# Optimization experiments

Measured on AMD Instinct MI355X. Metric: run time of the kernel, lower is better.

Reference implementation:

```python
import jax, jax.numpy as jnp
import numpy as np

B, N, F = 8, 1024, 256
OUT, REL = 256, 16
NADJ = 7  # ((2 relations + consecutive) * 2 for backward) + self link


def setup_inputs() -> dict:
    key = jax.random.key(0)
    k0, k1, k2, k3, k4 = jax.random.split(key, 5)
    features = jax.random.normal(k0, (B, N, F), dtype=jnp.float32)
    A1 = jax.random.uniform(k1, (B, N, N), dtype=jnp.float32)
    A2 = jax.random.uniform(k2, (B, N, N), dtype=jnp.float32)
    # learned params: one (F+REL, OUT) weight per adjacency matrix, edge embeddings init 'ones', bias (N, OUT)
    W = jax.random.normal(k3, (NADJ, F + REL, OUT), dtype=jnp.float32) * 0.05
    W_edges = jnp.ones((NADJ, REL), dtype=jnp.float32)
    b = jax.random.uniform(k4, (N, OUT), dtype=jnp.float32, minval=-0.05, maxval=0.05)
    return {"features": features, "A1": A1, "A2": A2, "W": W, "W_edges": W_edges, "b": b}


def reference(features, A1, A2, W, W_edges, b):
    # eye = A[0] * zeros(N) + eye(N)  -> batch-broadcast identity [B,N,N]
    eye = jnp.zeros_like(A1) + jnp.eye(N, dtype=A1.dtype)
    # original rolls along axis 0 (batch) of the broadcast identity (faithful replication)
    shifted = jnp.roll(eye, 1, axis=0)
    A_fwd = [A1, A2, shifted]                      # relations + consecutive link
    A_list = A_fwd + [jnp.swapaxes(a, 1, 2) for a in A_fwd]  # backward links
    A_list.append(eye)                             # self links
    A = jnp.stack(A_list, axis=0)                  # [R,B,N,N]

    # concat(features, tile(W_edges[r])) @ W[r] == features @ W[r][:F] + W_edges[r] @ W[r][F:]
    HW = jnp.einsum('bnf,rfo->rbno', features, W[:, :F]) \
         + jnp.einsum('rd,rdo->ro', W_edges, W[:, F:])[:, None, None, :]  # [R,B,N,OUT]
    AHW = jnp.einsum('rbnm,rbmo->rbno', A, HW)     # batched adjacency matmul
    out = jnp.max(AHW, axis=0) + b                 # max-aggregate over relations, add bias
    return out                                     # activation = linear
```

## Files before the change

kernel.cpp:

```cpp
#include <hip/hip_runtime.h>
#include <hip/hip_bf16.h>

#define B_ 8
#define N_ 1024
#define F_ 256
#define OUT_ 256
#define REL_ 16
#define NADJ_ 7

typedef __attribute__((ext_vector_type(8))) _Float16 f16x8;
typedef __attribute__((ext_vector_type(2))) _Float16 f16x2;
typedef __attribute__((ext_vector_type(4))) float f32x4;

__device__ __forceinline__ void gll16(const _Float16* g, _Float16* l) {
    __builtin_amdgcn_global_load_lds(
        (const __attribute__((address_space(1))) void*)g,
        (__attribute__((address_space(3))) void*)l, 16, 0, 0);
}

__constant__ const int c_perm[7] = {0, 1, 3, 4, 2, 5, 6};

__global__ __launch_bounds__(256) void prep_kernel(const float* __restrict__ W,
                                                   const float* __restrict__ We,
                                                   const float* __restrict__ feat,
                                                   float* __restrict__ cb,
                                                   _Float16* __restrict__ WTp,
                                                   _Float16* __restrict__ Fe) {
    int bid = blockIdx.x, tid = threadIdx.x;
    if (bid < 7) {
        int idx = bid * 256 + tid;
        int j = idx / OUT_, o = idx % OUT_;
        int r = c_perm[j];
        const float* Wr = W + (size_t)r * (F_ + REL_) * OUT_;
        float s = 0.f;
#pragma unroll
        for (int d = 0; d < REL_; ++d) s += We[r * REL_ + d] * Wr[(F_ + d) * OUT_ + o];
        cb[idx] = s;
    } else if (bid < 1799) {
        int idx = (bid - 7) * 256 + tid;
        int j = idx >> 16, rem = idx & 65535, o = rem >> 8, f = rem & 255;
        int r = c_perm[j];
        WTp[idx] = (_Float16)W[((size_t)r * (F_ + REL_) + f) * OUT_ + o];
    } else {
        int i = (bid - 1799) * 256 + tid;
        size_t base = (size_t)i * 8;
        float4 a = *(const float4*)(feat + base);
        float4 b = *(const float4*)(feat + base + 4);
        f16x8 v = {(_Float16)a.x, (_Float16)a.y, (_Float16)a.z, (_Float16)a.w,
                   (_Float16)b.x, (_Float16)b.y, (_Float16)b.z, (_Float16)b.w};
        *(f16x8*)(Fe + base) = v;
    }
}

__global__ __launch_bounds__(256) void hw7_kernel(const _Float16* __restrict__ Fe,
                                                  const _Float16* __restrict__ WTp,
                                                  const float* __restrict__ cb,
                                                  _Float16* __restrict__ HWT,
                                                  _Float16* __restrict__ HWN) {
    __shared__ _Float16 S[8192];
    const int bid = blockIdx.x, tid = threadIdx.x;
    const int z = bid / 128, rem = bid % 128, bx = rem & 63, by = rem >> 6;
    const bool tr = (z < 4);
    const _Float16* A  = tr ? (WTp + (size_t)z * 65536) : Fe;
    const _Float16* Bt = tr ? Fe : (WTp + (size_t)z * 65536);
    const int m0 = (tr ? by : bx) * 128;
    const int n0 = (tr ? bx : by) * 128;
    _Float16* As = S;
    _Float16* Bs = S + 4096;
    const int wave = tid >> 6, lane = tid & 63, lm = lane & 15, q = lane >> 4;
    const int wr = (wave >> 1) * 64, wc = (wave & 1) * 64;
    const int srow = tid >> 2, sk = (tid & 3) * 8;
    const _Float16* ga0 = A + (size_t)(m0 + srow) * F_ + sk;
    const _Float16* ga1 = ga0 + (size_t)64 * F_;
    const _Float16* gb0 = Bt + (size_t)(n0 + srow) * F_ + sk;
    const _Float16* gb1 = gb0 + (size_t)64 * F_;
    _Float16* la0 = As + tid * 8;
    _Float16* la1 = As + 2048 + tid * 8;
    _Float16* lb0 = Bs + tid * 8;
    _Float16* lb1 = Bs + 2048 + tid * 8;

    f32x4 acc[4][4] = {};
    for (int k0 = 0; k0 < F_; k0 += 32) {
        gll16(ga0 + k0, la0);
        gll16(ga1 + k0, la1);
        gll16(gb0 + k0, lb0);
        gll16(gb1 + k0, lb1);
        __syncthreads();
        f16x8 af[4], bf[4];
#pragma unroll
        for (int i = 0; i < 4; ++i) af[i] = *(const f16x8*)(As + (wr + i * 16 + lm) * 32 + q * 8);
#pragma unroll
        for (int j = 0; j < 4; ++j) bf[j] = *(const f16x8*)(Bs + (wc + j * 16 + lm) * 32 + q * 8);
#pragma unroll
        for (int i = 0; i < 4; ++i)
#pragma unroll
            for (int j = 0; j < 4; ++j)
                acc[i][j] = __builtin_amdgcn_mfma_f32_16x16x32_f16(af[i], bf[j], acc[i][j], 0, 0, 0);
        __syncthreads();
    }
    const float* cbz = cb + (size_t)z * 256;
    if (tr) {
        _Float16* C = HWT + (size_t)z * ((size_t)256 * 8192);
#pragma unroll
        for (int i = 0; i < 4; ++i)
#pragma unroll
            for (int j = 0; j < 4; ++j)
#pragma unroll
                for (int g = 0; g < 4; ++g) {
                    int row = wr + i * 16 + q * 4 + g;
                    int col = wc + j * 16 + lm;
                    float v = acc[i][j][g] + cbz[m0 + row];
                    C[(size_t)(m0 + row) * 8192 + (n0 + col)] = (_Float16)v;
                }
    } else {
        _Float16* C = HWN + (size_t)(z - 4) * ((size_t)8192 * 256);
#pragma unroll
        for (int i = 0; i < 4; ++i)
#pragma unroll
            for (int j = 0; j < 4; ++j)
#pragma unroll
                for (int g = 0; g < 4; ++g) {
                    int row = wr + i * 16 + q * 4 + g;
                    int col = wc + j * 16 + lm;
                    float v = acc[i][j][g] + cbz[n0 + col];
                    C[(size_t)(m0 + row) * 256 + (n0 + col)] = (_Float16)v;
                }
    }
}

__global__ __launch_bounds__(256) void p2_kernel(const float* __restrict__ A1,
                                                 const float* __restrict__ A2,
                                                 const _Float16* __restrict__ HWT,
                                                 _Float16* __restrict__ AHW) {
    __shared__ _Float16 As[128 * 32];
    __shared__ _Float16 Bs[128 * 32];
    const int d = blockIdx.x;
    const int member = (d >> 3) & 1;
    const int p = (d & 7) | ((d >> 4) << 3);
    const int mt = p & 7, zz = p >> 3;
    const int rr = zz >> 3, b = zz & 7;
    const _Float16* Bt = HWT + (size_t)rr * (256 * 8192) + (size_t)b * 1024;
    _Float16* C = AHW + (size_t)rr * (8 * 262144) + (size_t)b * 262144;
    const int m0 = mt * 128, n0 = member * 128;
    const int tid = threadIdx.x;
    const int wave = tid >> 6, lane = tid & 63, lm = lane & 15, q = lane >> 4;
    const int wr = (wave >> 1) * 64, wc = (wave & 1) * 64;
    const int srow = tid >> 2, sk = (tid & 3) * 8;
    const _Float16* gb0 = Bt + (size_t)(n0 + srow) * 8192 + sk;
    const _Float16* gb1 = gb0 + (size_t)64 * 8192;
    _Float16* lb0 = Bs + tid * 8;
    _Float16* lb1 = Bs + 2048 + tid * 8;
    const int swv = (tid >> 6) & 3;
    _Float16* la0 = As + (tid >> 2) * 32 + (((tid & 3) ^ swv) * 8);
    _Float16* la1 = la0 + 2048;

    const float* Ag = ((rr & 1) ? A2 : A1) + (size_t)b * N_ * N_;
    f32x4 acc[4][4] = {};
    if (rr < 2) {
        const float* Ag0 = Ag + (size_t)(m0 + srow) * N_ + sk;
        const float* Ag1 = Ag0 + (size_t)64 * N_;
        float4 pa0 = *(const float4*)(Ag0);
        float4 pa1 = *(const float4*)(Ag0 + 4);
        float4 pb0 = *(const float4*)(Ag1);
        float4 pb1 = *(const float4*)(Ag1 + 4);
        for (int k0 = 0; k0 < N_; k0 += 32) {
            f16x8 v0 = {(_Float16)pa0.x, (_Float16)pa0.y, (_Float16)pa0.z, (_Float16)pa0.w,
                        (_Float16)pa1.x, (_Float16)pa1.y, (_Float16)pa1.z, (_Float16)pa1.w};
            f16x8 v1 = {(_Float16)pb0.x, (_Float16)pb0.y, (_Float16)pb0.z, (_Float16)pb0.w,
                        (_Float16)pb1.x, (_Float16)pb1.y, (_Float16)pb1.z, (_Float16)pb1.w};
            *(f16x8*)la0 = v0;
            *(f16x8*)la1 = v1;
            gll16(gb0 + k0, lb0);
            gll16(gb1 + k0, lb1);
            if (k0 + 32 < N_) {
                pa0 = *(const float4*)(Ag0 + k0 + 32);
                pa1 = *(const float4*)(Ag0 + k0 + 36);
                pb0 = *(const float4*)(Ag1 + k0 + 32);
                pb1 = *(const float4*)(Ag1 + k0 + 36);
            }
            __syncthreads();
            f16x8 af[4], bf[4];
#pragma unroll
            for (int i = 0; i < 4; ++i)
                af[i] = *(const f16x8*)(As + (wr + i * 16 + lm) * 32 + ((q ^ i) * 8));
#pragma unroll
            for (int j = 0; j < 4; ++j)
                bf[j] = *(const f16x8*)(Bs + (wc + j * 16 + lm) * 32 + q * 8);
#pragma unroll
            for (int i = 0; i < 4; ++i)
#pragma unroll
                for (int j = 0; j < 4; ++j)
                    acc[i][j] = __builtin_amdgcn_mfma_f32_16x16x32_f16(af[i], bf[j], acc[i][j], 0, 0, 0);
            __syncthreads();
        }
    } else {
        const int kk = (tid >> 4) * 2, ms = (tid & 15) * 8;
        const int sw = (ms >> 4) & 3;
        _Float16* wp = As + ms * 32 + (kk ^ (sw << 3));
        const float* ga = Ag + (size_t)kk * N_ + m0 + ms;
        float4 pa0 = *(const float4*)(ga);
        float4 pa1 = *(const float4*)(ga + 4);
        float4 pb0 = *(const float4*)(ga + N_);
        float4 pb1 = *(const float4*)(ga + N_ + 4);
        for (int k0 = 0; k0 < N_; k0 += 32) {
            f16x2 w;
            w = f16x2{(_Float16)pa0.x, (_Float16)pb0.x}; *(f16x2*)(wp + 0 * 32) = w;
            w = f16x2{(_Float16)pa0.y, (_Float16)pb0.y}; *(f16x2*)(wp + 1 * 32) = w;
            w = f16x2{(_Float16)pa0.z, (_Float16)pb0.z}; *(f16x2*)(wp + 2 * 32) = w;
            w = f16x2{(_Float16)pa0.w, (_Float16)pb0.w}; *(f16x2*)(wp + 3 * 32) = w;
            w = f16x2{(_Float16)pa1.x, (_Float16)pb1.x}; *(f16x2*)(wp + 4 * 32) = w;
            w = f16x2{(_Float16)pa1.y, (_Float16)pb1.y}; *(f16x2*)(wp + 5 * 32) = w;
            w = f16x2{(_Float16)pa1.z, (_Float16)pb1.z}; *(f16x2*)(wp + 6 * 32) = w;
            w = f16x2{(_Float16)pa1.w, (_Float16)pb1.w}; *(f16x2*)(wp + 7 * 32) = w;
            gll16(gb0 + k0, lb0);
            gll16(gb1 + k0, lb1);
            if (k0 + 32 < N_) {
                ga += (size_t)32 * N_;
                pa0 = *(const float4*)(ga);
                pa1 = *(const float4*)(ga + 4);
                pb0 = *(const float4*)(ga + N_);
                pb1 = *(const float4*)(ga + N_ + 4);
            }
            __syncthreads();
            f16x8 af[4], bf[4];
#pragma unroll
            for (int i = 0; i < 4; ++i)
                af[i] = *(const f16x8*)(As + (wr + i * 16 + lm) * 32 + ((q ^ i) * 8));
#pragma unroll
            for (int j = 0; j < 4; ++j)
                bf[j] = *(const f16x8*)(Bs + (wc + j * 16 + lm) * 32 + q * 8);
#pragma unroll
            for (int i = 0; i < 4; ++i)
#pragma unroll
                for (int j = 0; j < 4; ++j)
                    acc[i][j] = __builtin_amdgcn_mfma_f32_16x16x32_f16(af[i], bf[j], acc[i][j], 0, 0, 0);
            __syncthreads();
        }
    }
#pragma unroll
    for (int i = 0; i < 4; ++i)
#pragma unroll
        for (int j = 0; j < 4; ++j)
#pragma unroll
            for (int g = 0; g < 4; ++g) {
                int row = wr + i * 16 + q * 4 + g;
                int col = wc + j * 16 + lm;
                C[(size_t)(m0 + row) * 256 + (n0 + col)] = (_Float16)acc[i][j][g];
            }
}

__global__ __launch_bounds__(256) void max_kernel(const _Float16* __restrict__ AHW,
                                                  const _Float16* __restrict__ HWN,
                                                  const float* __restrict__ bias,
                                                  float* __restrict__ out) {
    size_t i = ((size_t)blockIdx.x * 256 + threadIdx.x) * 8;
    const size_t slab = (size_t)B_ * N_ * OUT_;
    float m[8];
    f16x8 v = *(const f16x8*)(AHW + i);
#pragma unroll
    for (int e = 0; e < 8; ++e) m[e] = (float)v[e];
#pragma unroll
    for (int rr = 1; rr < 4; ++rr) {
        f16x8 w = *(const f16x8*)(AHW + rr * slab + i);
#pragma unroll
        for (int e = 0; e < 8; ++e) m[e] = fmaxf(m[e], (float)w[e]);
    }
#pragma unroll
    for (int j = 0; j < 3; ++j) {
        f16x8 w = *(const f16x8*)(HWN + j * slab + i);
#pragma unroll
        for (int e = 0; e < 8; ++e) m[e] = fmaxf(m[e], (float)w[e]);
    }
    size_t bidx = i & ((size_t)N_ * OUT_ - 1);
    float4 b0 = *(const float4*)(bias + bidx);
    float4 b1 = *(const float4*)(bias + bidx + 4);
    float4 o0 = {m[0] + b0.x, m[1] + b0.y, m[2] + b0.z, m[3] + b0.w};
    float4 o1 = {m[4] + b1.x, m[5] + b1.y, m[6] + b1.z, m[7] + b1.w};
    *(float4*)(out + i) = o0;
    *(float4*)(out + i + 4) = o1;
}

__global__ void cbias_kernel(const float* __restrict__ W, const float* __restrict__ We,
                             float* __restrict__ c) {
    int idx = blockIdx.x * 256 + threadIdx.x;
    if (idx >= NADJ_ * OUT_) return;
    int r = idx / OUT_, o = idx % OUT_;
    const float* Wr = W + (size_t)r * (F_ + REL_) * OUT_;
    float s = 0.f;
#pragma unroll
    for (int d = 0; d < REL_; ++d) s += We[r * REL_ + d] * Wr[(F_ + d) * OUT_ + o];
    c[idx] = s;
}

__global__ __launch_bounds__(256) void hw_kernel(const float* __restrict__ feat,
                                                 const float* __restrict__ W,
                                                 const float* __restrict__ cb,
                                                 _Float16* __restrict__ HWb) {
    __shared__ _Float16 As[64][32];
    __shared__ _Float16 Bs[64][32];
    const int mt = blockIdx.x, ct = blockIdx.y;
    const int tid = threadIdx.x, wave = tid >> 6, lane = tid & 63;
    const int r = (ct * 64) / OUT_;
    const int o0 = (ct * 64) % OUT_;
    const float* Bg = W + (size_t)r * (F_ + REL_) * OUT_ + o0;
    const int m0 = mt * 64;
    const int lm = lane & 15, q = lane >> 4;
    f32x4 acc[4] = {};
    for (int k0 = 0; k0 < F_; k0 += 32) {
        {
            int seg = (tid & 3) * 8, m = tid >> 2;
            const float* src = feat + (size_t)(m0 + m) * F_ + k0 + seg;
#pragma unroll
            for (int j = 0; j < 8; ++j) As[m][seg + j] = (_Float16)src[j];
        }
        {
            int kk = tid >> 3, ns = (tid & 7) * 8;
            const float* src = Bg + (size_t)(k0 + kk) * OUT_ + ns;
#pragma unroll
            for (int j = 0; j < 8; ++j) Bs[ns + j][kk] = (_Float16)src[j];
        }
        __syncthreads();
        f16x8 a = *(const f16x8*)&As[wave * 16 + lm][q * 8];
#pragma unroll
        for (int c4 = 0; c4 < 4; ++c4) {
            f16x8 b = *(const f16x8*)&Bs[c4 * 16 + lm][q * 8];
            acc[c4] = __builtin_amdgcn_mfma_f32_16x16x32_f16(a, b, acc[c4], 0, 0, 0);
        }
        __syncthreads();
    }
#pragma unroll
    for (int c4 = 0; c4 < 4; ++c4)
#pragma unroll
        for (int g = 0; g < 4; ++g) {
            int row = wave * 16 + (lane >> 4) * 4 + g;
            int col = c4 * 16 + lm;
            float v = acc[c4][g] + cb[r * OUT_ + o0 + col];
            HWb[((size_t)r * B_ * N_ + m0 + row) * OUT_ + o0 + col] = (_Float16)v;
        }
}

__global__ __launch_bounds__(256) void agg_kernel(const float* __restrict__ A1,
                                                  const float* __restrict__ A2,
                                                  const _Float16* __restrict__ HWb,
                                                  const float* __restrict__ bias,
                                                  float* __restrict__ out) {
    __shared__ _Float16 As[64][32];
    __shared__ _Float16 Bs[64][32];
    const int b = blockIdx.z, nt = blockIdx.y, ot = blockIdx.x;
    const int tid = threadIdx.x, wave = tid >> 6, lane = tid & 63;
    const int n0 = nt * 64, o0 = ot * 64;
    const int lm = lane & 15, q = lane >> 4;
    const size_t rstride = (size_t)B_ * N_ * OUT_;
    f32x4 mx[4];
#pragma unroll
    for (int i = 0; i < 4; ++i) mx[i] = f32x4{-1e30f, -1e30f, -1e30f, -1e30f};
#pragma unroll 1
    for (int rr = 0; rr < 4; ++rr) {
        const float* Ag = ((rr & 1) ? A2 : A1) + (size_t)b * N_ * N_;
        const bool tr = (rr >= 2);
        const int r = (rr < 2) ? rr : rr + 1;
        const _Float16* Bg = HWb + (size_t)r * rstride + (size_t)b * N_ * OUT_ + o0;
        f32x4 acc[4] = {};
        for (int k0 = 0; k0 < N_; k0 += 32) {
            if (!tr) {
                int seg = (tid & 3) * 8, m = tid >> 2;
                const float* src = Ag + (size_t)(n0 + m) * N_ + k0 + seg;
#pragma unroll
                for (int j = 0; j < 8; ++j) As[m][seg + j] = (_Float16)src[j];
            } else {
                int kk = tid >> 3, ms = (tid & 7) * 8;
                const float* src = Ag + (size_t)(k0 + kk) * N_ + n0 + ms;
#pragma unroll
                for (int j = 0; j < 8; ++j) As[ms + j][kk] = (_Float16)src[j];
            }
            {
                int kk = tid >> 3, ns = (tid & 7) * 8;
                const _Float16* src = Bg + (size_t)(k0 + kk) * OUT_ + ns;
#pragma unroll
                for (int j = 0; j < 8; ++j) Bs[ns + j][kk] = src[j];
            }
            __syncthreads();
            f16x8 a = *(const f16x8*)&As[wave * 16 + lm][q * 8];
#pragma unroll
            for (int c4 = 0; c4 < 4; ++c4) {
                f16x8 bb = *(const f16x8*)&Bs[c4 * 16 + lm][q * 8];
                acc[c4] = __builtin_amdgcn_mfma_f32_16x16x32_f16(a, bb, acc[c4], 0, 0, 0);
            }
            __syncthreads();
        }
#pragma unroll
        for (int c4 = 0; c4 < 4; ++c4)
#pragma unroll
            for (int g = 0; g < 4; ++g) mx[c4][g] = fmaxf(mx[c4][g], acc[c4][g]);
    }
#pragma unroll
    for (int c4 = 0; c4 < 4; ++c4)
#pragma unroll
        for (int g = 0; g < 4; ++g) {
            int row = wave * 16 + (lane >> 4) * 4 + g;
            int col = c4 * 16 + lm;
            size_t pos = ((size_t)b * N_ + n0 + row) * OUT_ + o0 + col;
            float v = mx[c4][g];
            v = fmaxf(v, (float)HWb[2 * rstride + pos]);
            v = fmaxf(v, (float)HWb[5 * rstride + pos]);
            v = fmaxf(v, (float)HWb[6 * rstride + pos]);
            out[pos] = v + bias[((size_t)(n0 + row)) * OUT_ + o0 + col];
        }
}

extern "C" void kernel_launch(void* const* d_in, const int* in_sizes, int n_in,
                              void* d_out, int out_size, void* d_ws, size_t ws_size,
                              hipStream_t stream) {
    const float* feat = (const float*)d_in[0];
    const float* A1   = (const float*)d_in[1];
    const float* A2   = (const float*)d_in[2];
    const float* W    = (const float*)d_in[3];
    const float* We   = (const float*)d_in[4];
    const float* bias = (const float*)d_in[5];
    float* out = (float*)d_out;

    const size_t OFF_CB   = 0;
    const size_t OFF_WT   = 8192;
    const size_t OFF_FE   = 1048576;
    const size_t OFF_HWT  = 5242880;
    const size_t OFF_HWN  = 22020096;
    const size_t OFF_AHW  = 34603008;
    const size_t WS_NEEDED = 51380224;

    if (ws_size >= WS_NEEDED) {
        float*    cbp = (float*)((char*)d_ws + OFF_CB);
        _Float16* WTp = (_Float16*)((char*)d_ws + OFF_WT);
        _Float16* Fe  = (_Float16*)((char*)d_ws + OFF_FE);
        _Float16* HWT = (_Float16*)((char*)d_ws + OFF_HWT);
        _Float16* HWN = (_Float16*)((char*)d_ws + OFF_HWN);
        _Float16* AHW = (_Float16*)((char*)d_ws + OFF_AHW);

        prep_kernel<<<2823, 256, 0, stream>>>(W, We, feat, cbp, WTp, Fe);
        hw7_kernel<<<896, 256, 0, stream>>>(Fe, WTp, cbp, HWT, HWN);
        p2_kernel<<<512, 256, 0, stream>>>(A1, A2, HWT, AHW);
        max_kernel<<<1024, 256, 0, stream>>>(AHW, HWN, bias, out);
    } else {
        float* cb = (float*)d_ws;
        _Float16* HWb = (_Float16*)((char*)d_ws + 8192);
        cbias_kernel<<<7, 256, 0, stream>>>(W, We, cb);
        hw_kernel<<<dim3(128, 28), 256, 0, stream>>>(feat, W, cb, HWb);
        agg_kernel<<<dim3(4, 16, 8), 256, 0, stream>>>(A1, A2, HWb, bias, out);
    }
}
```

Baseline: 188.7 us.

## Split-K the adjacency matmul into two halves and sum partials in max kernel

The p2 aggregation GEMM is split along K into two 512-wide halves, doubling the grid from 512 to 1024 blocks so the GPU's compute units are better filled. Each iteration now stages 64 K-columns in two LDS sub-buffers, halving the number of barriers per unit of work. Partial results go to a second AHW slab, and the max kernel adds the two partials before taking the max, which costs extra fp16 workspace traffic and rounds each partial to fp16 separately. The workspace requirement grows, so the fast path falls back to the slow path if the workspace is too small.

```diff
diff --git a/kernel.cpp b/kernel.cpp
--- a/kernel.cpp
+++ b/kernel.cpp
@@ -9,6 +9,7 @@
 #define NADJ_ 7
 
 typedef __attribute__((ext_vector_type(8))) _Float16 f16x8;
+typedef __attribute__((ext_vector_type(4))) _Float16 f16x4;
 typedef __attribute__((ext_vector_type(2))) _Float16 f16x2;
 typedef __attribute__((ext_vector_type(4))) float f32x4;
 
@@ -16,6 +17,11 @@
     __builtin_amdgcn_global_load_lds(
         (const __attribute__((address_space(1))) void*)g,
         (__attribute__((address_space(3))) void*)l, 16, 0, 0);
+}
+
+__device__ __forceinline__ f16x8 cvt8(float4 a, float4 b) {
+    return f16x8{(_Float16)a.x, (_Float16)a.y, (_Float16)a.z, (_Float16)a.w,
+                 (_Float16)b.x, (_Float16)b.y, (_Float16)b.z, (_Float16)b.w};
 }
 
 __constant__ const int c_perm[7] = {0, 1, 3, 4, 2, 5, 6};
@@ -46,9 +52,7 @@
         size_t base = (size_t)i * 8;
         float4 a = *(const float4*)(feat + base);
         float4 b = *(const float4*)(feat + base + 4);
-        f16x8 v = {(_Float16)a.x, (_Float16)a.y, (_Float16)a.z, (_Float16)a.w,
-                   (_Float16)b.x, (_Float16)b.y, (_Float16)b.z, (_Float16)b.w};
-        *(f16x8*)(Fe + base) = v;
+        *(f16x8*)(Fe + base) = cvt8(a, b);
     }
 }
 
@@ -132,108 +136,123 @@
                                                  const float* __restrict__ A2,
                                                  const _Float16* __restrict__ HWT,
                                                  _Float16* __restrict__ AHW) {
-    __shared__ _Float16 As[128 * 32];
-    __shared__ _Float16 Bs[128 * 32];
+    __shared__ _Float16 As[2 * 4096];
+    __shared__ _Float16 Bs[2 * 4096];
     const int d = blockIdx.x;
-    const int member = (d >> 3) & 1;
-    const int p = (d & 7) | ((d >> 4) << 3);
-    const int mt = p & 7, zz = p >> 3;
+    const int xcd = d & 7, slot = d >> 3;
+    const int Ghi = xcd + 8 * (slot >> 4);
+    const int member = (slot >> 3) & 1;
+    const int mt = slot & 7;
+    const int kh = Ghi & 1;
+    const int zz = Ghi >> 1;
     const int rr = zz >> 3, b = zz & 7;
+
+    const size_t slab = (size_t)B_ * N_ * OUT_;
     const _Float16* Bt = HWT + (size_t)rr * (256 * 8192) + (size_t)b * 1024;
-    _Float16* C = AHW + (size_t)rr * (8 * 262144) + (size_t)b * 262144;
-    const int m0 = mt * 128, n0 = member * 128;
+    _Float16* C = AHW + (size_t)kh * (4 * slab) + (size_t)rr * slab + (size_t)b * (N_ * OUT_);
+    const int m0 = mt * 128, n0 = member * 128, kbase = kh * 512;
     const int tid = threadIdx.x;
     const int wave = tid >> 6, lane = tid & 63, lm = lane & 15, q = lane >> 4;
     const int wr = (wave >> 1) * 64, wc = (wave & 1) * 64;
     const int srow = tid >> 2, sk = (tid & 3) * 8;
-    const _Float16* gb0 = Bt + (size_t)(n0 + srow) * 8192 + sk;
+    const _Float16* gb0 = Bt + (size_t)(n0 + srow) * 8192 + kbase + sk;
     const _Float16* gb1 = gb0 + (size_t)64 * 8192;
     _Float16* lb0 = Bs + tid * 8;
     _Float16* lb1 = Bs + 2048 + tid * 8;
-    const int swv = (tid >> 6) & 3;
-    _Float16* la0 = As + (tid >> 2) * 32 + (((tid & 3) ^ swv) * 8);
-    _Float16* la1 = la0 + 2048;
+    _Float16* la0 = As + srow * 32 + (((tid & 3) ^ ((tid >> 6) & 3)) * 8);
 
     const float* Ag = ((rr & 1) ? A2 : A1) + (size_t)b * N_ * N_;
     f32x4 acc[4][4] = {};
-    if (rr < 2) {
-        const float* Ag0 = Ag + (size_t)(m0 + srow) * N_ + sk;
-        const float* Ag1 = Ag0 + (size_t)64 * N_;
-        float4 pa0 = *(const float4*)(Ag0);
-        float4 pa1 = *(const float4*)(Ag0 + 4);
-        float4 pb0 = *(const float4*)(Ag1);
-        float4 pb1 = *(const float4*)(Ag1 + 4);
-        for (int k0 = 0; k0 < N_; k0 += 32) {
-            f16x8 v0 = {(_Float16)pa0.x, (_Float16)pa0.y, (_Float16)pa0.z, (_Float16)pa0.w,
-                        (_Float16)pa1.x, (_Float16)pa1.y, (_Float16)pa1.z, (_Float16)pa1.w};
-            f16x8 v1 = {(_Float16)pb0.x, (_Float16)pb0.y, (_Float16)pb0.z, (_Float16)pb0.w,
-                        (_Float16)pb1.x, (_Float16)pb1.y, (_Float16)pb1.z, (_Float16)pb1.w};
-            *(f16x8*)la0 = v0;
-            *(f16x8*)la1 = v1;
-            gll16(gb0 + k0, lb0);
-            gll16(gb1 + k0, lb1);
-            if (k0 + 32 < N_) {
-                pa0 = *(const float4*)(Ag0 + k0 + 32);
-                pa1 = *(const float4*)(Ag0 + k0 + 36);
-                pb0 = *(const float4*)(Ag1 + k0 + 32);
-                pb1 = *(const float4*)(Ag1 + k0 + 36);
-            }
-            __syncthreads();
+
+    auto domfma = [&]() {
+#pragma unroll
+        for (int u2 = 0; u2 < 2; ++u2) {
+            const _Float16* Au = As + u2 * 4096;
+            const _Float16* Bu = Bs + u2 * 4096;
             f16x8 af[4], bf[4];
 #pragma unroll
             for (int i = 0; i < 4; ++i)
-                af[i] = *(const f16x8*)(As + (wr + i * 16 + lm) * 32 + ((q ^ i) * 8));
+                af[i] = *(const f16x8*)(Au + (wr + i * 16 + lm) * 32 + ((q ^ i) * 8));
 #pragma unroll
             for (int j = 0; j < 4; ++j)
-                bf[j] = *(const f16x8*)(Bs + (wc + j * 16 + lm) * 32 + q * 8);
+                bf[j] = *(const f16x8*)(Bu + (wc + j * 16 + lm) * 32 + q * 8);
 #pragma unroll
             for (int i = 0; i < 4; ++i)
 #pragma unroll
                 for (int j = 0; j < 4; ++j)
                     acc[i][j] = __builtin_amdgcn_mfma_f32_16x16x32_f16(af[i], bf[j], acc[i][j], 0, 0, 0);
+        }
+    };
+
+    if (rr < 2) {
+        const float* Ag0 = Ag + (size_t)(m0 + srow) * N_ + kbase + sk;
+        const float* Ag1 = Ag0 + (size_t)64 * N_;
+        float4 r0a = *(const float4*)(Ag0);
+        float4 r0b = *(const float4*)(Ag0 + 4);
+        float4 r1a = *(const float4*)(Ag0 + 32);
+        float4 r1b = *(const float4*)(Ag0 + 36);
+        float4 r2a = *(const float4*)(Ag1);
+        float4 r2b = *(const float4*)(Ag1 + 4);
+        float4 r3a = *(const float4*)(Ag1 + 32);
+        float4 r3b = *(const float4*)(Ag1 + 36);
+        for (int t = 0; t < 8; ++t) {
+            gll16(gb0 + t * 64, lb0);
+            gll16(gb0 + t * 64 + 32, lb0 + 4096);
+            gll16(gb1 + t * 64, lb1);
+            gll16(gb1 + t * 64 + 32, lb1 + 4096);
+            *(f16x8*)(la0)        = cvt8(r0a, r0b);
+            *(f16x8*)(la0 + 4096) = cvt8(r1a, r1b);
+            *(f16x8*)(la0 + 2048) = cvt8(r2a, r2b);
+            *(f16x8*)(la0 + 6144) = cvt8(r3a, r3b);
+            if (t < 7) {
+                const float* p0 = Ag0 + (t + 1) * 64;
+                const float* p1 = Ag1 + (t + 1) * 64;
+                r0a = *(const float4*)(p0);      r0b = *(const float4*)(p0 + 4);
+                r1a = *(const float4*)(p0 + 32); r1b = *(const float4*)(p0 + 36);
+                r2a = *(const float4*)(p1);      r2b = *(const float4*)(p1 + 4);
+                r3a = *(const float4*)(p1 + 32); r3b = *(const float4*)(p1 + 36);
+            }
+            __syncthreads();
+            domfma();
             __syncthreads();
         }
     } else {
-        const int kk = (tid >> 4) * 2, ms = (tid & 15) * 8;
-        const int sw = (ms >> 4) & 3;
-        _Float16* wp = As + ms * 32 + (kk ^ (sw << 3));
-        const float* ga = Ag + (size_t)kk * N_ + m0 + ms;
-        float4 pa0 = *(const float4*)(ga);
-        float4 pa1 = *(const float4*)(ga + 4);
-        float4 pb0 = *(const float4*)(ga + N_);
-        float4 pb1 = *(const float4*)(ga + N_ + 4);
-        for (int k0 = 0; k0 < N_; k0 += 32) {
-            f16x2 w;
-            w = f16x2{(_Float16)pa0.x, (_Float16)pb0.x}; *(f16x2*)(wp + 0 * 32) = w;
-            w = f16x2{(_Float16)pa0.y, (_Float16)pb0.y}; *(f16x2*)(wp + 1 * 32) = w;
-            w = f16x2{(_Float16)pa0.z, (_Float16)pb0.z}; *(f16x2*)(wp + 2 * 32) = w;
-            w = f16x2{(_Float16)pa0.w, (_Float16)pb0.w}; *(f16x2*)(wp + 3 * 32) = w;
-            w = f16x2{(_Float16)pa1.x, (_Float16)pb1.x}; *(f16x2*)(wp + 4 * 32) = w;
-            w = f16x2{(_Float16)pa1.y, (_Float16)pb1.y}; *(f16x2*)(wp + 5 * 32) = w;
-            w = f16x2{(_Float16)pa1.z, (_Float16)pb1.z}; *(f16x2*)(wp + 6 * 32) = w;
-            w = f16x2{(_Float16)pa1.w, (_Float16)pb1.w}; *(f16x2*)(wp + 7 * 32) = w;
-            gll16(gb0 + k0, lb0);
-            gll16(gb1 + k0, lb1);
-            if (k0 + 32 < N_) {
-                ga += (size_t)32 * N_;
-                pa0 = *(const float4*)(ga);
-                pa1 = *(const float4*)(ga + 4);
-                pb0 = *(const float4*)(ga + N_);
-                pb1 = *(const float4*)(ga + N_ + 4);
-            }
-            __syncthreads();
-            f16x8 af[4], bf[4];
-#pragma unroll
-            for (int i = 0; i < 4; ++i)
-                af[i] = *(const f16x8*)(As + (wr + i * 16 + lm) * 32 + ((q ^ i) * 8));
-#pragma unroll
-            for (int j = 0; j < 4; ++j)
-                bf[j] = *(const f16x8*)(Bs + (wc + j * 16 + lm) * 32 + q * 8);
-#pragma unroll
-            for (int i = 0; i < 4; ++i)
-#pragma unroll
-                for (int j = 0; j < 4; ++j)
-                    acc[i][j] = __builtin_amdgcn_mfma_f32_16x16x32_f16(af[i], bf[j], acc[i][j], 0, 0, 0);
+        const int kk4 = (tid >> 4) * 4;
+        const int ms = (tid & 15) * 8;
+        const int u = kk4 >> 5, kl = kk4 & 31;
+        const int tsw = ((ms >> 4) & 3) << 3;
+        _Float16* wp = As + u * 4096 + ms * 32 + (kl ^ tsw);
+        const float* gA = Ag + (size_t)(kbase + kk4) * N_ + m0 + ms;
+        float4 ra0 = *(const float4*)(gA);
+        float4 rb0 = *(const float4*)(gA + 4);
+        float4 ra1 = *(const float4*)(gA + N_);
+        float4 rb1 = *(const float4*)(gA + N_ + 4);
+        float4 ra2 = *(const float4*)(gA + 2 * N_);
+        float4 rb2 = *(const float4*)(gA + 2 * N_ + 4);
+        float4 ra3 = *(const float4*)(gA + 3 * N_);
+        float4 rb3 = *(const float4*)(gA + 3 * N_ + 4);
+        for (int t = 0; t < 8; ++t) {
+            gll16(gb0 + t * 64, lb0);
+            gll16(gb0 + t * 64 + 32, lb0 + 4096);
+            gll16(gb1 + t * 64, lb1);
+            gll16(gb1 + t * 64 + 32, lb1 + 4096);
+            *(f16x4*)(wp + 0 * 32) = f16x4{(_Float16)ra0.x, (_Float16)ra1.x, (_Float16)ra2.x, (_Float16)ra3.x};
+            *(f16x4*)(wp + 1 * 32) = f16x4{(_Float16)ra0.y, (_Float16)ra1.y, (_Float16)ra2.y, (_Float16)ra3.y};
+            *(f16x4*)(wp + 2 * 32) = f16x4{(_Float16)ra0.z, (_Float16)ra1.z, (_Float16)ra2.z, (_Float16)ra3.z};
+            *(f16x4*)(wp + 3 * 32) = f16x4{(_Float16)ra0.w, (_Float16)ra1.w, (_Float16)ra2.w, (_Float16)ra3.w};
+            *(f16x4*)(wp + 4 * 32) = f16x4{(_Float16)rb0.x, (_Float16)rb1.x, (_Float16)rb2.x, (_Float16)rb3.x};
+            *(f16x4*)(wp + 5 * 32) = f16x4{(_Float16)rb0.y, (_Float16)rb1.y, (_Float16)rb2.y, (_Float16)rb3.y};
+            *(f16x4*)(wp + 6 * 32) = f16x4{(_Float16)rb0.z, (_Float16)rb1.z, (_Float16)rb2.z, (_Float16)rb3.z};
+            *(f16x4*)(wp + 7 * 32) = f16x4{(_Float16)rb0.w, (_Float16)rb1.w, (_Float16)rb2.w, (_Float16)rb3.w};
+            if (t < 7) {
+                const float* p = gA + (size_t)(t + 1) * 64 * N_;
+                ra0 = *(const float4*)(p);          rb0 = *(const float4*)(p + 4);
+                ra1 = *(const float4*)(p + N_);     rb1 = *(const float4*)(p + N_ + 4);
+                ra2 = *(const float4*)(p + 2 * N_); rb2 = *(const float4*)(p + 2 * N_ + 4);
+                ra3 = *(const float4*)(p + 3 * N_); rb3 = *(const float4*)(p + 3 * N_ + 4);
+            }
+            __syncthreads();
+            domfma();
             __syncthreads();
         }
     }
@@ -255,15 +274,20 @@
                                                   float* __restrict__ out) {
     size_t i = ((size_t)blockIdx.x * 256 + threadIdx.x) * 8;
     const size_t slab = (size_t)B_ * N_ * OUT_;
+    const size_t HS = 4 * slab;
     float m[8];
-    f16x8 v = *(const f16x8*)(AHW + i);
-#pragma unroll
-    for (int e = 0; e < 8; ++e) m[e] = (float)v[e];
+    {
+        f16x8 v0 = *(const f16x8*)(AHW + i);
+        f16x8 v1 = *(const f16x8*)(AHW + HS + i);
+#pragma unroll
+        for (int e = 0; e < 8; ++e) m[e] = (float)v0[e] + (float)v1[e];
+    }
 #pragma unroll
     for (int rr = 1; rr < 4; ++rr) {
-        f16x8 w = *(const f16x8*)(AHW + rr * slab + i);
-#pragma unroll
-        for (int e = 0; e < 8; ++e) m[e] = fmaxf(m[e], (float)w[e]);
+        f16x8 v0 = *(const f16x8*)(AHW + rr * slab + i);
+        f16x8 v1 = *(const f16x8*)(AHW + HS + rr * slab + i);
+#pragma unroll
+        for (int e = 0; e < 8; ++e) m[e] = fmaxf(m[e], (float)v0[e] + (float)v1[e]);
     }
 #pragma unroll
     for (int j = 0; j < 3; ++j) {
@@ -425,7 +449,7 @@
     const size_t OFF_HWT  = 5242880;
     const size_t OFF_HWN  = 22020096;
     const size_t OFF_AHW  = 34603008;
-    const size_t WS_NEEDED = 51380224;
+    const size_t WS_NEEDED = 68157440;
 
     if (ws_size >= WS_NEEDED) {
         float*    cbp = (float*)((char*)d_ws + OFF_CB);
@@ -437,7 +461,7 @@
 
         prep_kernel<<<2823, 256, 0, stream>>>(W, We, feat, cbp, WTp, Fe);
         hw7_kernel<<<896, 256, 0, stream>>>(Fe, WTp, cbp, HWT, HWN);
-        p2_kernel<<<512, 256, 0, stream>>>(A1, A2, HWT, AHW);
+        p2_kernel<<<1024, 256, 0, stream>>>(A1, A2, HWT, AHW);
         max_kernel<<<1024, 256, 0, stream>>>(AHW, HWN, bias, out);
     } else {
         float* cb = (float*)d_ws;
```

New measurement: 174.5 us. 1.08x faster.

## Triple-buffer LDS with manual waitcnt pipelining in HW and adjacency GEMMs

Applied to the files above, without the earlier changes.

Both GEMM kernels now use three shared-memory stages, issuing global-to-LDS loads two K-steps ahead and synchronising with explicit s_waitcnt vmcnt plus a raw s_barrier instead of two __syncthreads per step. The goal is to overlap load latency with MFMA work. It also raises MFMA wave priority, changes the block-to-XCD mapping in p2 so the M tiles and both N halves of one relation/batch land on the same XCD, and widens the transposed A-load path to 4x4 f16x4 stores. The cost is triple LDS use, which may lower occupancy, and hand-tuned vmcnt counts that depend on exact instruction ordering.

```diff
diff --git a/kernel.cpp b/kernel.cpp
--- a/kernel.cpp
+++ b/kernel.cpp
@@ -9,7 +9,7 @@
 #define NADJ_ 7
 
 typedef __attribute__((ext_vector_type(8))) _Float16 f16x8;
-typedef __attribute__((ext_vector_type(2))) _Float16 f16x2;
+typedef __attribute__((ext_vector_type(4))) _Float16 f16x4;
 typedef __attribute__((ext_vector_type(4))) float f32x4;
 
 __device__ __forceinline__ void gll16(const _Float16* g, _Float16* l) {
@@ -17,6 +17,13 @@
         (const __attribute__((address_space(1))) void*)g,
         (__attribute__((address_space(3))) void*)l, 16, 0, 0);
 }
+
+__device__ __forceinline__ f16x8 cvt8(float4 a, float4 b) {
+    return f16x8{(_Float16)a.x, (_Float16)a.y, (_Float16)a.z, (_Float16)a.w,
+                 (_Float16)b.x, (_Float16)b.y, (_Float16)b.z, (_Float16)b.w};
+}
+
+#define MEMPIN() asm volatile("" ::: "memory")
 
 __constant__ const int c_perm[7] = {0, 1, 3, 4, 2, 5, 6};
 
@@ -46,9 +53,7 @@
         size_t base = (size_t)i * 8;
         float4 a = *(const float4*)(feat + base);
         float4 b = *(const float4*)(feat + base + 4);
-        f16x8 v = {(_Float16)a.x, (_Float16)a.y, (_Float16)a.z, (_Float16)a.w,
-                   (_Float16)b.x, (_Float16)b.y, (_Float16)b.z, (_Float16)b.w};
-        *(f16x8*)(Fe + base) = v;
+        *(f16x8*)(Fe + base) = cvt8(a, b);
     }
 }
 
@@ -57,7 +62,7 @@
                                                   const float* __restrict__ cb,
                                                   _Float16* __restrict__ HWT,
                                                   _Float16* __restrict__ HWN) {
-    __shared__ _Float16 S[8192];
+    __shared__ _Float16 S[3 * 8192];
     const int bid = blockIdx.x, tid = threadIdx.x;
     const int z = bid / 128, rem = bid % 128, bx = rem & 63, by = rem >> 6;
     const bool tr = (z < 4);
@@ -65,8 +70,6 @@
     const _Float16* Bt = tr ? Fe : (WTp + (size_t)z * 65536);
     const int m0 = (tr ? by : bx) * 128;
     const int n0 = (tr ? bx : by) * 128;
-    _Float16* As = S;
-    _Float16* Bs = S + 4096;
     const int wave = tid >> 6, lane = tid & 63, lm = lane & 15, q = lane >> 4;
     const int wr = (wave >> 1) * 64, wc = (wave & 1) * 64;
     const int srow = tid >> 2, sk = (tid & 3) * 8;
@@ -74,29 +77,55 @@
     const _Float16* ga1 = ga0 + (size_t)64 * F_;
     const _Float16* gb0 = Bt + (size_t)(n0 + srow) * F_ + sk;
     const _Float16* gb1 = gb0 + (size_t)64 * F_;
-    _Float16* la0 = As + tid * 8;
-    _Float16* la1 = As + 2048 + tid * 8;
-    _Float16* lb0 = Bs + tid * 8;
-    _Float16* lb1 = Bs + 2048 + tid * 8;
 
     f32x4 acc[4][4] = {};
-    for (int k0 = 0; k0 < F_; k0 += 32) {
-        gll16(ga0 + k0, la0);
-        gll16(ga1 + k0, la1);
-        gll16(gb0 + k0, lb0);
-        gll16(gb1 + k0, lb1);
-        __syncthreads();
-        f16x8 af[4], bf[4];
-#pragma unroll
-        for (int i = 0; i < 4; ++i) af[i] = *(const f16x8*)(As + (wr + i * 16 + lm) * 32 + q * 8);
-#pragma unroll
-        for (int j = 0; j < 4; ++j) bf[j] = *(const f16x8*)(Bs + (wc + j * 16 + lm) * 32 + q * 8);
-#pragma unroll
-        for (int i = 0; i < 4; ++i)
-#pragma unroll
-            for (int j = 0; j < 4; ++j)
-                acc[i][j] = __builtin_amdgcn_mfma_f32_16x16x32_f16(af[i], bf[j], acc[i][j], 0, 0, 0);
-        __syncthreads();
+    const int NT = 8;
+
+    {
+        gll16(ga0, S + tid * 8);
+        gll16(ga1, S + 2048 + tid * 8);
+        gll16(gb0, S + 4096 + tid * 8);
+        gll16(gb1, S + 6144 + tid * 8);
+        MEMPIN();
+        gll16(ga0 + 32, S + 8192 + tid * 8);
+        gll16(ga1 + 32, S + 8192 + 2048 + tid * 8);
+        gll16(gb0 + 32, S + 8192 + 4096 + tid * 8);
+        gll16(gb1 + 32, S + 8192 + 6144 + tid * 8);
+        asm volatile("s_waitcnt vmcnt(4)" ::: "memory");
+        __builtin_amdgcn_s_barrier();
+    }
+    int cs = 0, ns = 1, fs = 2;
+    for (int t = 0; t < NT; ++t) {
+        if (t + 2 < NT) {
+            const int k = (t + 2) * 32;
+            _Float16* sb = S + fs * 8192;
+            gll16(ga0 + k, sb + tid * 8);
+            gll16(ga1 + k, sb + 2048 + tid * 8);
+            gll16(gb0 + k, sb + 4096 + tid * 8);
+            gll16(gb1 + k, sb + 6144 + tid * 8);
+        }
+        {
+            const _Float16* Au = S + cs * 8192;
+            const _Float16* Bu = Au + 4096;
+            f16x8 af[4], bf[4];
+#pragma unroll
+            for (int i = 0; i < 4; ++i) af[i] = *(const f16x8*)(Au + (wr + i * 16 + lm) * 32 + q * 8);
+#pragma unroll
+            for (int j = 0; j < 4; ++j) bf[j] = *(const f16x8*)(Bu + (wc + j * 16 + lm) * 32 + q * 8);
+            __builtin_amdgcn_s_setprio(1);
+#pragma unroll
+            for (int i = 0; i < 4; ++i)
+#pragma unroll
+                for (int j = 0; j < 4; ++j)
+                    acc[i][j] = __builtin_amdgcn_mfma_f32_16x16x32_f16(af[i], bf[j], acc[i][j], 0, 0, 0);
+            __builtin_amdgcn_s_setprio(0);
+        }
+        if (t + 1 < NT) {
+            if (t + 2 < NT) asm volatile("s_waitcnt vmcnt(4)" ::: "memory");
+            else            asm volatile("s_waitcnt vmcnt(0)" ::: "memory");
+            __builtin_amdgcn_s_barrier();
+        }
+        int tmp = cs; cs = ns; ns = fs; fs = tmp;
     }
     const float* cbz = cb + (size_t)z * 256;
     if (tr) {
@@ -132,15 +161,18 @@
                                                  const float* __restrict__ A2,
                                                  const _Float16* __restrict__ HWT,
                                                  _Float16* __restrict__ AHW) {
-    __shared__ _Float16 As[128 * 32];
-    __shared__ _Float16 Bs[128 * 32];
+    __shared__ _Float16 As[3 * 4096];
+    __shared__ _Float16 Bs[3 * 4096];
     const int d = blockIdx.x;
-    const int member = (d >> 3) & 1;
-    const int p = (d & 7) | ((d >> 4) << 3);
-    const int mt = p & 7, zz = p >> 3;
+    const int xcd = d & 7, slot = d >> 3;
+    const int zz = xcd + 8 * (slot >> 4);
+    const int member = (slot >> 3) & 1;
+    const int mt = slot & 7;
     const int rr = zz >> 3, b = zz & 7;
+
+    const size_t slab = (size_t)B_ * N_ * OUT_;
     const _Float16* Bt = HWT + (size_t)rr * (256 * 8192) + (size_t)b * 1024;
-    _Float16* C = AHW + (size_t)rr * (8 * 262144) + (size_t)b * 262144;
+    _Float16* C = AHW + (size_t)rr * slab + (size_t)b * (N_ * OUT_);
     const int m0 = mt * 128, n0 = member * 128;
     const int tid = threadIdx.x;
     const int wave = tid >> 6, lane = tid & 63, lm = lane & 15, q = lane >> 4;
@@ -148,93 +180,147 @@
     const int srow = tid >> 2, sk = (tid & 3) * 8;
     const _Float16* gb0 = Bt + (size_t)(n0 + srow) * 8192 + sk;
     const _Float16* gb1 = gb0 + (size_t)64 * 8192;
-    _Float16* lb0 = Bs + tid * 8;
-    _Float16* lb1 = Bs + 2048 + tid * 8;
-    const int swv = (tid >> 6) & 3;
-    _Float16* la0 = As + (tid >> 2) * 32 + (((tid & 3) ^ swv) * 8);
-    _Float16* la1 = la0 + 2048;
 
     const float* Ag = ((rr & 1) ? A2 : A1) + (size_t)b * N_ * N_;
     f32x4 acc[4][4] = {};
+    const int NT = 32;
+
+    auto mfma_step = [&](int st) {
+        const _Float16* Au = As + st * 4096;
+        const _Float16* Bu = Bs + st * 4096;
+        f16x8 af[4], bf[4];
+#pragma unroll
+        for (int i = 0; i < 4; ++i)
+            af[i] = *(const f16x8*)(Au + (wr + i * 16 + lm) * 32 + ((q ^ i) * 8));
+#pragma unroll
+        for (int j = 0; j < 4; ++j)
+            bf[j] = *(const f16x8*)(Bu + (wc + j * 16 + lm) * 32 + q * 8);
+        __builtin_amdgcn_s_setprio(1);
+#pragma unroll
+        for (int i = 0; i < 4; ++i)
+#pragma unroll
+            for (int j = 0; j < 4; ++j)
+                acc[i][j] = __builtin_amdgcn_mfma_f32_16x16x32_f16(af[i], bf[j], acc[i][j], 0, 0, 0);
+        __builtin_amdgcn_s_setprio(0);
+    };
+
     if (rr < 2) {
         const float* Ag0 = Ag + (size_t)(m0 + srow) * N_ + sk;
         const float* Ag1 = Ag0 + (size_t)64 * N_;
-        float4 pa0 = *(const float4*)(Ag0);
-        float4 pa1 = *(const float4*)(Ag0 + 4);
-        float4 pb0 = *(const float4*)(Ag1);
-        float4 pb1 = *(const float4*)(Ag1 + 4);
-        for (int k0 = 0; k0 < N_; k0 += 32) {
-            f16x8 v0 = {(_Float16)pa0.x, (_Float16)pa0.y, (_Float16)pa0.z, (_Float16)pa0.w,
-                        (_Float16)pa1.x, (_Float16)pa1.y, (_Float16)pa1.z, (_Float16)pa1.w};
-            f16x8 v1 = {(_Float16)pb0.x, (_Float16)pb0.y, (_Float16)pb0.z, (_Float16)pb0.w,
-                        (_Float16)pb1.x, (_Float16)pb1.y, (_Float16)pb1.z, (_Float16)pb1.w};
-            *(f16x8*)la0 = v0;
-            *(f16x8*)la1 = v1;
-            gll16(gb0 + k0, lb0);
-            gll16(gb1 + k0, lb1);
-            if (k0 + 32 < N_) {
-                pa0 = *(const float4*)(Ag0 + k0 + 32);
-                pa1 = *(const float4*)(Ag0 + k0 + 36);
-                pb0 = *(const float4*)(Ag1 + k0 + 32);
-                pb1 = *(const float4*)(Ag1 + k0 + 36);
-            }
-            __syncthreads();
-            f16x8 af[4], bf[4];
-#pragma unroll
-            for (int i = 0; i < 4; ++i)
-                af[i] = *(const f16x8*)(As + (wr + i * 16 + lm) * 32 + ((q ^ i) * 8));
-#pragma unroll
-            for (int j = 0; j < 4; ++j)
-                bf[j] = *(const f16x8*)(Bs + (wc + j * 16 + lm) * 32 + q * 8);
-#pragma unroll
-            for (int i = 0; i < 4; ++i)
-#pragma unroll
-                for (int j = 0; j < 4; ++j)
-                    acc[i][j] = __builtin_amdgcn_mfma_f32_16x16x32_f16(af[i], bf[j], acc[i][j], 0, 0, 0);
-            __syncthreads();
+        const int sx = ((tid & 3) ^ ((tid >> 6) & 3)) * 8;
+        float4 p0, p1, p2, p3;
+        {
+            float4 q0 = *(const float4*)(Ag0);
+            float4 q1 = *(const float4*)(Ag0 + 4);
+            float4 q2 = *(const float4*)(Ag1);
+            float4 q3 = *(const float4*)(Ag1 + 4);
+            *(f16x8*)(As + srow * 32 + sx) = cvt8(q0, q1);
+            *(f16x8*)(As + 2048 + srow * 32 + sx) = cvt8(q2, q3);
+            MEMPIN();
+            gll16(gb0, Bs + tid * 8);
+            gll16(gb1, Bs + 2048 + tid * 8);
+            MEMPIN();
+            p0 = *(const float4*)(Ag0 + 32);
+            p1 = *(const float4*)(Ag0 + 36);
+            p2 = *(const float4*)(Ag1 + 32);
+            p3 = *(const float4*)(Ag1 + 36);
+            MEMPIN();
+            gll16(gb0 + 32, Bs + 4096 + tid * 8);
+            gll16(gb1 + 32, Bs + 4096 + 2048 + tid * 8);
+            asm volatile("s_waitcnt vmcnt(6)" ::: "memory");
+            asm volatile("s_waitcnt lgkmcnt(0)" ::: "memory");
+            __builtin_amdgcn_s_barrier();
+        }
+        int cs = 0, ns = 1, fs = 2;
+        for (int t = 0; t < NT; ++t) {
+            if (t + 1 < NT) {
+                _Float16* la = As + ns * 4096 + srow * 32 + sx;
+                *(f16x8*)(la) = cvt8(p0, p1);
+                *(f16x8*)(la + 2048) = cvt8(p2, p3);
+            }
+            MEMPIN();
+            if (t + 2 < NT) {
+                const int k2 = (t + 2) * 32;
+                p0 = *(const float4*)(Ag0 + k2);
+                p1 = *(const float4*)(Ag0 + k2 + 4);
+                p2 = *(const float4*)(Ag1 + k2);
+                p3 = *(const float4*)(Ag1 + k2 + 4);
+                MEMPIN();
+                gll16(gb0 + k2, Bs + fs * 4096 + tid * 8);
+                gll16(gb1 + k2, Bs + fs * 4096 + 2048 + tid * 8);
+            }
+            mfma_step(cs);
+            if (t + 1 < NT) {
+                if (t + 2 < NT) asm volatile("s_waitcnt vmcnt(6)" ::: "memory");
+                else            asm volatile("s_waitcnt vmcnt(0)" ::: "memory");
+                asm volatile("s_waitcnt lgkmcnt(0)" ::: "memory");
+                __builtin_amdgcn_s_barrier();
+            }
+            int tmp = cs; cs = ns; ns = fs; fs = tmp;
         }
     } else {
-        const int kk = (tid >> 4) * 2, ms = (tid & 15) * 8;
-        const int sw = (ms >> 4) & 3;
-        _Float16* wp = As + ms * 32 + (kk ^ (sw << 3));
-        const float* ga = Ag + (size_t)kk * N_ + m0 + ms;
-        float4 pa0 = *(const float4*)(ga);
-        float4 pa1 = *(const float4*)(ga + 4);
-        float4 pb0 = *(const float4*)(ga + N_);
-        float4 pb1 = *(const float4*)(ga + N_ + 4);
-        for (int k0 = 0; k0 < N_; k0 += 32) {
-            f16x2 w;
-            w = f16x2{(_Float16)pa0.x, (_Float16)pb0.x}; *(f16x2*)(wp + 0 * 32) = w;
-            w = f16x2{(_Float16)pa0.y, (_Float16)pb0.y}; *(f16x2*)(wp + 1 * 32) = w;
-            w = f16x2{(_Float16)pa0.z, (_Float16)pb0.z}; *(f16x2*)(wp + 2 * 32) = w;
-            w = f16x2{(_Float16)pa0.w, (_Float16)pb0.w}; *(f16x2*)(wp + 3 * 32) = w;
-            w = f16x2{(_Float16)pa1.x, (_Float16)pb1.x}; *(f16x2*)(wp + 4 * 32) = w;
-            w = f16x2{(_Float16)pa1.y, (_Float16)pb1.y}; *(f16x2*)(wp + 5 * 32) = w;
-            w = f16x2{(_Float16)pa1.z, (_Float16)pb1.z}; *(f16x2*)(wp + 6 * 32) = w;
-            w = f16x2{(_Float16)pa1.w, (_Float16)pb1.w}; *(f16x2*)(wp + 7 * 32) = w;
-            gll16(gb0 + k0, lb0);
-            gll16(gb1 + k0, lb1);
-            if (k0 + 32 < N_) {
-                ga += (size_t)32 * N_;
-                pa0 = *(const float4*)(ga);
-                pa1 = *(const float4*)(ga + 4);
-                pb0 = *(const float4*)(ga + N_);
-                pb1 = *(const float4*)(ga + N_ + 4);
-            }
-            __syncthreads();
-            f16x8 af[4], bf[4];
-#pragma unroll
-            for (int i = 0; i < 4; ++i)
-                af[i] = *(const f16x8*)(As + (wr + i * 16 + lm) * 32 + ((q ^ i) * 8));
-#pragma unroll
-            for (int j = 0; j < 4; ++j)
-                bf[j] = *(const f16x8*)(Bs + (wc + j * 16 + lm) * 32 + q * 8);
-#pragma unroll
-            for (int i = 0; i < 4; ++i)
-#pragma unroll
-                for (int j = 0; j < 4; ++j)
-                    acc[i][j] = __builtin_amdgcn_mfma_f32_16x16x32_f16(af[i], bf[j], acc[i][j], 0, 0, 0);
-            __syncthreads();
+        const int kk4 = (tid >> 5) * 4;
+        const int ms4 = (tid & 31) * 4;
+        const int tsw = ((ms4 >> 4) & 3) << 3;
+        const int wof = ms4 * 32 + (kk4 ^ tsw);
+        const float* gA0 = Ag + (size_t)kk4 * N_ + m0 + ms4;
+        float4 r0, r1, r2, r3;
+        {
+            float4 q0 = *(const float4*)(gA0);
+            float4 q1 = *(const float4*)(gA0 + N_);
+            float4 q2 = *(const float4*)(gA0 + 2 * N_);
+            float4 q3 = *(const float4*)(gA0 + 3 * N_);
+            _Float16* wp = As + wof;
+            *(f16x4*)(wp + 0 * 32) = f16x4{(_Float16)q0.x, (_Float16)q1.x, (_Float16)q2.x, (_Float16)q3.x};
+            *(f16x4*)(wp + 1 * 32) = f16x4{(_Float16)q0.y, (_Float16)q1.y, (_Float16)q2.y, (_Float16)q3.y};
+            *(f16x4*)(wp + 2 * 32) = f16x4{(_Float16)q0.z, (_Float16)q1.z, (_Float16)q2.z, (_Float16)q3.z};
+            *(f16x4*)(wp + 3 * 32) = f16x4{(_Float16)q0.w, (_Float16)q1.w, (_Float16)q2.w, (_Float16)q3.w};
+            MEMPIN();
+            gll16(gb0, Bs + tid * 8);
+            gll16(gb1, Bs + 2048 + tid * 8);
+            MEMPIN();
+            const float* p = gA0 + (size_t)32 * N_;
+            r0 = *(const float4*)(p);
+            r1 = *(const float4*)(p + N_);
+            r2 = *(const float4*)(p + 2 * N_);
+            r3 = *(const float4*)(p + 3 * N_);
+            MEMPIN();
+            gll16(gb0 + 32, Bs + 4096 + tid * 8);
+            gll16(gb1 + 32, Bs + 4096 + 2048 + tid * 8);
+            asm volatile("s_waitcnt vmcnt(6)" ::: "memory");
+            asm volatile("s_waitcnt lgkmcnt(0)" ::: "memory");
+            __builtin_amdgcn_s_barrier();
+        }
+        const float* gp = gA0 + (size_t)64 * N_;
+        int cs = 0, ns = 1, fs = 2;
+        for (int t = 0; t < NT; ++t) {
+            if (t + 1 < NT) {
+                _Float16* wp = As + ns * 4096 + wof;
+                *(f16x4*)(wp + 0 * 32) = f16x4{(_Float16)r0.x, (_Float16)r1.x, (_Float16)r2.x, (_Float16)r3.x};
+                *(f16x4*)(wp + 1 * 32) = f16x4{(_Float16)r0.y, (_Float16)r1.y, (_Float16)r2.y, (_Float16)r3.y};
+                *(f16x4*)(wp + 2 * 32) = f16x4{(_Float16)r0.z, (_Float16)r1.z, (_Float16)r2.z, (_Float16)r3.z};
+                *(f16x4*)(wp + 3 * 32) = f16x4{(_Float16)r0.w, (_Float16)r1.w, (_Float16)r2.w, (_Float16)r3.w};
+            }
+            MEMPIN();
+            if (t + 2 < NT) {
+                r0 = *(const float4*)(gp);
+                r1 = *(const float4*)(gp + N_);
+                r2 = *(const float4*)(gp + 2 * N_);
+                r3 = *(const float4*)(gp + 3 * N_);
+                gp += (size_t)32 * N_;
+                MEMPIN();
+                const int k2 = (t + 2) * 32;
+                gll16(gb0 + k2, Bs + fs * 4096 + tid * 8);
+                gll16(gb1 + k2, Bs + fs * 4096 + 2048 + tid * 8);
+            }
+            mfma_step(cs);
+            if (t + 1 < NT) {
+                if (t + 2 < NT) asm volatile("s_waitcnt vmcnt(6)" ::: "memory");
+                else            asm volatile("s_waitcnt vmcnt(0)" ::: "memory");
+                asm volatile("s_waitcnt lgkmcnt(0)" ::: "memory");
+                __builtin_amdgcn_s_barrier();
+            }
+            int tmp = cs; cs = ns; ns = fs; fs = tmp;
         }
     }
 #pragma unroll
```

New measurement: 174.4 us. 7.5% less time.
